# Kernel tuning notes

Hardware: AMD Instinct MI355X
Metric: run time of the kernel (lower is better)

## Reference

```python
import jax, jax.numpy as jnp
import numpy as np

EMBED_DIM = 1024
ATTN_DIM = 128
B, S = 4, 2048


def setup_inputs() -> dict:
    key = jax.random.key(0)
    k1, k2, k3, k4 = jax.random.split(key, 4)
    embedded = jax.random.normal(k1, (B, S, EMBED_DIM), dtype=jnp.float32)
    # torch nn.Linear weights are [out_features, in_features]
    scale = 1.0 / np.sqrt(EMBED_DIM)
    Wk = jax.random.uniform(k2, (ATTN_DIM, EMBED_DIM), dtype=jnp.float32, minval=-scale, maxval=scale)
    Wq = jax.random.uniform(k3, (ATTN_DIM, EMBED_DIM), dtype=jnp.float32, minval=-scale, maxval=scale)
    Wv = jax.random.uniform(k4, (ATTN_DIM, EMBED_DIM), dtype=jnp.float32, minval=-scale, maxval=scale)
    return {"embedded": embedded, "Wk": Wk, "Wq": Wq, "Wv": Wv}


def reference(embedded, Wk, Wq, Wv):
    # projections (no bias): x @ W.T
    k = jnp.einsum('bse,ae->bsa', embedded, Wk)  # [B,S,A]
    q = jnp.einsum('bse,ae->bsa', embedded, Wq)
    v = jnp.einsum('bse,ae->bsa', embedded, Wv)
    ad = k.shape[-1]
    scores = jnp.einsum('bqa,bka->bqk', q, k) / jnp.sqrt(jnp.float32(ad))  # [B,S,S]
    causal = jnp.tril(jnp.ones((scores.shape[1], scores.shape[1]), dtype=bool))
    scores = jnp.where(causal, scores, -jnp.inf)
    probs = jax.nn.softmax(scores, axis=-1)
    out = jnp.einsum('bqk,bka->bqa', probs, v)
    return jnp.round(out, 4)
```

## Files before the change

kernel.cpp:

```cpp
#include <hip/hip_runtime.h>
#include <hip/hip_bf16.h>
#include <math.h>

#define B 4
#define S 2048
#define E 1024
#define A 128
#define CHUNK 256
#define NCHMAX 8

typedef __attribute__((ext_vector_type(8))) short short8;
typedef __attribute__((ext_vector_type(4))) float floatx4;

static __device__ __forceinline__ short f2bf(float f) {
  union { float f; unsigned u; } c;
  c.f = f;
  unsigned r = (c.u + 0x7fffu + ((c.u >> 16) & 1u)) >> 16;
  return (short)r;
}
static __device__ __forceinline__ unsigned f2bf2(float x, float y) {
  __hip_bfloat162 h = __float22bfloat162_rn(float2{x, y});
  union { __hip_bfloat162 h; unsigned u; } c;
  c.h = h;
  return c.u;
}

__global__ __launch_bounds__(256) void wconv(
    const float* __restrict__ Wq,
    const float* __restrict__ Wk,
    const float* __restrict__ Wv,
    short* __restrict__ Wbf) {
  const int which = blockIdx.y;
  const float* Wp = (which == 0) ? Wq : (which == 1) ? Wk : Wv;
  short* o = Wbf + (size_t)which * A * E;
  const int f = blockIdx.x * 256 + threadIdx.x;
  const float4 v = *(const float4*)&Wp[(size_t)f * 4];
  uint2 p; p.x = f2bf2(v.x, v.y); p.y = f2bf2(v.z, v.w);
  *(uint2*)&o[(size_t)f * 4] = p;
}

#define PJ 72
__global__ __launch_bounds__(256) void proj_gemm(
    const float* __restrict__ X,
    const short* __restrict__ Wbf,
    short* __restrict__ Qbf,
    short* __restrict__ Kbf,
    short* __restrict__ Vt) {
  __shared__ short As[64 * PJ];
  __shared__ short Bs[128 * PJ];

  const int m0 = blockIdx.x * 64;
  const int which = blockIdx.y;
  const short* Wpb = Wbf + (size_t)which * A * E;

  const int tid = threadIdx.x;
  const int wave = tid >> 6;
  const int lane = tid & 63;
  const int mh = wave & 1;
  const int nh = wave >> 1;
  const int l16 = lane & 15;
  const int quad = lane >> 4;

  int arow[4], ac4[4], brow[4], bc8[4];
#pragma unroll
  for (int i = 0; i < 4; ++i) {
    const int fa = tid + i * 256;
    arow[i] = fa >> 4; ac4[i] = fa & 15;
    const int fb = tid + i * 256;
    brow[i] = fb >> 3; bc8[i] = fb & 7;
  }

  floatx4 acc[2][4] = {};
  float4 aplf[4];
  short8 bplf[4];

#pragma unroll
  for (int i = 0; i < 4; ++i) {
    aplf[i] = *(const float4*)&X[(size_t)(m0 + arow[i]) * E + ac4[i] * 4];
    bplf[i] = *(const short8*)&Wpb[(size_t)brow[i] * E + bc8[i] * 8];
  }

  for (int k0 = 0; k0 < E; k0 += 64) {
    __syncthreads();
#pragma unroll
    for (int i = 0; i < 4; ++i) {
      uint2 p; p.x = f2bf2(aplf[i].x, aplf[i].y); p.y = f2bf2(aplf[i].z, aplf[i].w);
      *(uint2*)&As[arow[i] * PJ + ac4[i] * 4] = p;
      *(short8*)&Bs[brow[i] * PJ + bc8[i] * 8] = bplf[i];
    }
    __syncthreads();

    if (k0 + 64 < E) {
#pragma unroll
      for (int i = 0; i < 4; ++i) {
        aplf[i] = *(const float4*)&X[(size_t)(m0 + arow[i]) * E + (k0 + 64) + ac4[i] * 4];
        bplf[i] = *(const short8*)&Wpb[(size_t)brow[i] * E + (k0 + 64) + bc8[i] * 8];
      }
    }

    short8 afr[2][2], bfr[4][2];
#pragma unroll
    for (int ms = 0; ms < 2; ++ms)
#pragma unroll
      for (int ks = 0; ks < 2; ++ks)
        afr[ms][ks] = *(const short8*)&As[(mh * 32 + ms * 16 + l16) * PJ + ks * 32 + quad * 8];
#pragma unroll
    for (int nt = 0; nt < 4; ++nt)
#pragma unroll
      for (int ks = 0; ks < 2; ++ks)
        bfr[nt][ks] = *(const short8*)&Bs[(nh * 64 + nt * 16 + l16) * PJ + ks * 32 + quad * 8];

#pragma unroll
    for (int ms = 0; ms < 2; ++ms)
#pragma unroll
      for (int nt = 0; nt < 4; ++nt)
#pragma unroll
        for (int ks = 0; ks < 2; ++ks)
          acc[ms][nt] = __builtin_amdgcn_mfma_f32_16x16x32_bf16(
              afr[ms][ks], bfr[nt][ks], acc[ms][nt], 0, 0, 0);
  }

  const float qscale = 0.08838834764831845f;
#pragma unroll
  for (int ms = 0; ms < 2; ++ms) {
#pragma unroll
    for (int nt = 0; nt < 4; ++nt) {
      const int n = nh * 64 + nt * 16 + l16;
      const int mbase = m0 + mh * 32 + ms * 16 + quad * 4;
      if (which == 2) {
        const int b = mbase >> 11, s = mbase & (S - 1);
        short4 p;
        p.x = f2bf(acc[ms][nt][0]); p.y = f2bf(acc[ms][nt][1]);
        p.z = f2bf(acc[ms][nt][2]); p.w = f2bf(acc[ms][nt][3]);
        *(short4*)&Vt[((size_t)b * A + n) * S + s] = p;
      } else {
        short* Outp = (which == 0) ? Qbf : Kbf;
        const float sc = (which == 0) ? qscale : 1.0f;
#pragma unroll
        for (int r = 0; r < 4; ++r)
          Outp[(size_t)(mbase + r) * A + n] = f2bf(acc[ms][nt][r] * sc);
      }
    }
  }
}

#define LK 132
#define LV 68
__global__ __launch_bounds__(256) void attn_part(
    const short* __restrict__ Qbf,
    const short* __restrict__ Kbf,
    const short* __restrict__ Vt,
    float* __restrict__ Opart,
    float* __restrict__ Lpart) {
  __shared__ short Ks[64 * LK];
  __shared__ short Vs[128 * LV];
  __shared__ short Ps[4][16 * LV];

  const int rev = (int)gridDim.x - 1 - (int)blockIdx.x;
  const int qt = rev >> 3;
  const int chunk = rev & 7;
  const int b = qt >> 5;
  const int q0 = (qt & 31) << 6;
  const int nk = q0 + 64;
  const int kstart = chunk * CHUNK;
  if (kstart >= nk) return;
  const int kend = min(kstart + CHUNK, nk);

  const int tid = threadIdx.x;
  const int wave = tid >> 6;
  const int lane = tid & 63;
  const int l16 = lane & 15;
  const int quad = lane >> 4;

  int krow[4], kc8[4], vrow[4], vc8[4];
#pragma unroll
  for (int i = 0; i < 4; ++i) {
    const int f = tid + i * 256;
    krow[i] = f >> 4; kc8[i] = f & 15;
    vrow[i] = f >> 3; vc8[i] = f & 7;
  }

  short8 qfr[4];
  {
    const size_t qrow = (size_t)(b * S + q0 + wave * 16 + l16);
#pragma unroll
    for (int ks = 0; ks < 4; ++ks)
      qfr[ks] = *(const short8*)&Qbf[qrow * A + ks * 32 + quad * 8];
  }

  float l_acc[4] = {0.f, 0.f, 0.f, 0.f};
  floatx4 oacc[8] = {};

  const int myrow = q0 + wave * 16 + quad * 4;
  const short* Kbase = Kbf + (size_t)b * S * A;
  const short* Vbase = Vt + (size_t)b * A * S;

  short8 kplf[4], vplf[4];
#pragma unroll
  for (int i = 0; i < 4; ++i) {
    kplf[i] = *(const short8*)&Kbase[(size_t)(kstart + krow[i]) * A + kc8[i] * 8];
    vplf[i] = *(const short8*)&Vbase[(size_t)vrow[i] * S + kstart + vc8[i] * 8];
  }

  for (int j0 = kstart; j0 < kend; j0 += 64) {
    __syncthreads();
#pragma unroll
    for (int i = 0; i < 4; ++i) {
      *(short8*)&Ks[krow[i] * LK + kc8[i] * 8] = kplf[i];
      *(short8*)&Vs[vrow[i] * LV + vc8[i] * 8] = vplf[i];
    }
    __syncthreads();

    if (j0 + 64 < kend) {
#pragma unroll
      for (int i = 0; i < 4; ++i) {
        kplf[i] = *(const short8*)&Kbase[(size_t)(j0 + 64 + krow[i]) * A + kc8[i] * 8];
        vplf[i] = *(const short8*)&Vbase[(size_t)vrow[i] * S + j0 + 64 + vc8[i] * 8];
      }
    }

    floatx4 sc[4];
#pragma unroll
    for (int nt = 0; nt < 4; ++nt) {
      floatx4 c = {};
#pragma unroll
      for (int ks = 0; ks < 4; ++ks) {
        const short8 bfr = *(const short8*)&Ks[(nt * 16 + l16) * LK + ks * 32 + quad * 8];
        c = __builtin_amdgcn_mfma_f32_16x16x32_bf16(qfr[ks], bfr, c, 0, 0, 0);
      }
      sc[nt] = c;
    }

#pragma unroll
    for (int nt = 0; nt < 4; ++nt) {
      const int key = j0 + nt * 16 + l16;
#pragma unroll
      for (int r = 0; r < 4; ++r) {
        const float p = (key > myrow + r) ? 0.f : __expf(sc[nt][r]);
        sc[nt][r] = p;
        l_acc[r] += p;
      }
    }

#pragma unroll
    for (int nt = 0; nt < 4; ++nt)
#pragma unroll
      for (int r = 0; r < 4; ++r)
        Ps[wave][(quad * 4 + r) * LV + nt * 16 + l16] = f2bf(sc[nt][r]);

    short8 pfr[2];
#pragma unroll
    for (int ks = 0; ks < 2; ++ks)
      pfr[ks] = *(const short8*)&Ps[wave][l16 * LV + ks * 32 + quad * 8];

#pragma unroll
    for (int nt = 0; nt < 8; ++nt) {
#pragma unroll
      for (int ks = 0; ks < 2; ++ks) {
        const short8 vfr = *(const short8*)&Vs[(nt * 16 + l16) * LV + ks * 32 + quad * 8];
        oacc[nt] = __builtin_amdgcn_mfma_f32_16x16x32_bf16(pfr[ks], vfr, oacc[nt], 0, 0, 0);
      }
    }
  }

  const int slot = qt * NCHMAX + chunk;
  float* op = Opart + (size_t)slot * 64 * 128;
  const int lr = wave * 16 + quad * 4;
#pragma unroll
  for (int nt = 0; nt < 8; ++nt)
#pragma unroll
    for (int r = 0; r < 4; ++r)
      op[(lr + r) * 128 + nt * 16 + l16] = oacc[nt][r];

#pragma unroll
  for (int r = 0; r < 4; ++r) {
    float l = l_acc[r];
    l += __shfl_xor(l, 1);
    l += __shfl_xor(l, 2);
    l += __shfl_xor(l, 4);
    l += __shfl_xor(l, 8);
    if (l16 == 0) Lpart[slot * 64 + lr + r] = l;
  }
}

__global__ __launch_bounds__(256) void attn_reduce(
    const float* __restrict__ Opart,
    const float* __restrict__ Lpart,
    float* __restrict__ Out) {
  const int qt = blockIdx.x;
  const int b = qt >> 5;
  const int q0 = (qt & 31) << 6;
  const int nch = (q0 + 64 + CHUNK - 1) / CHUNK;

  const int tid = threadIdx.x;
  const int lr = tid >> 2;
  const int c0 = (tid & 3) * 32;

  float ltot = 0.f;
  for (int c = 0; c < nch; ++c) ltot += Lpart[(qt * NCHMAX + c) * 64 + lr];
  const float inv = 1.f / ltot;

  float4 acc[8] = {};
  for (int c = 0; c < nch; ++c) {
    const float4* op = (const float4*)
        (Opart + ((size_t)(qt * NCHMAX + c) * 64 + lr) * 128 + c0);
#pragma unroll
    for (int i = 0; i < 8; ++i) {
      const float4 v = op[i];
      acc[i].x += v.x; acc[i].y += v.y; acc[i].z += v.z; acc[i].w += v.w;
    }
  }

  float4* o = (float4*)(Out + (size_t)(b * S + q0 + lr) * A + c0);
#pragma unroll
  for (int i = 0; i < 8; ++i) {
    float4 v = acc[i];
    v.x *= inv; v.y *= inv; v.z *= inv; v.w *= inv;
    o[i] = v;
  }
}

extern "C" void kernel_launch(void* const* d_in, const int* in_sizes, int n_in,
                              void* d_out, int out_size, void* d_ws, size_t ws_size,
                              hipStream_t stream) {
  const float* X  = (const float*)d_in[0];
  const float* Wk = (const float*)d_in[1];
  const float* Wq = (const float*)d_in[2];
  const float* Wv = (const float*)d_in[3];
  float* Out = (float*)d_out;

  const size_t qkv_elems = (size_t)B * S * A;
  short* Qbf = (short*)d_ws;
  short* Kbf = Qbf + qkv_elems;
  short* Vt  = Kbf + qkv_elems;
  float* Opart = (float*)(Vt + qkv_elems);
  float* Lpart = Opart + (size_t)1024 * 64 * 128;
  short* Wbf = (short*)(Lpart + (size_t)1024 * 64);

  wconv<<<dim3(A * E / 4 / 256, 3), 256, 0, stream>>>(Wq, Wk, Wv, Wbf);
  dim3 pgrid(B * S / 64, 3);
  proj_gemm<<<pgrid, 256, 0, stream>>>(X, Wbf, Qbf, Kbf, Vt);
  attn_part<<<(B * S / 64) * NCHMAX, 256, 0, stream>>>(Qbf, Kbf, Vt, Opart, Lpart);
  attn_reduce<<<B * S / 64, 256, 0, stream>>>(Opart, Lpart, Out);
}
```

Before: 131.5 us.

## Fuse split-K reduction into attention via last-block atomic counter; stage Q/K stores through LDS

Removes the separate attn_reduce kernel. Each attention chunk block increments a per-query-tile atomic counter, and the last block to finish sums the partial outputs and normalizes them. The projection GEMM now writes Q and K by staging the tile in shared memory, so the global stores become coalesced 16-byte writes instead of scattered 2-byte ones. The cost is an extra memset launch, threadfences and atomics, and a serialized reduction tail inside one block per tile.

New measurement: 361.4 us. +174.8%, slower.

```diff
diff --git a/kernel.cpp b/kernel.cpp
--- a/kernel.cpp
+++ b/kernel.cpp
@@ -40,14 +40,17 @@
 }
 
 #define PJ 72
+#define CN 130
 __global__ __launch_bounds__(256) void proj_gemm(
     const float* __restrict__ X,
     const short* __restrict__ Wbf,
     short* __restrict__ Qbf,
     short* __restrict__ Kbf,
     short* __restrict__ Vt) {
-  __shared__ short As[64 * PJ];
-  __shared__ short Bs[128 * PJ];
+  __shared__ __align__(16) char smem[27648];
+  short* As = (short*)smem;
+  short* Bs = (short*)(smem + 9216);
+  short* Cs = (short*)smem;
 
   const int m0 = blockIdx.x * 64;
   const int which = blockIdx.y;
@@ -121,25 +124,39 @@
   }
 
   const float qscale = 0.08838834764831845f;
-#pragma unroll
-  for (int ms = 0; ms < 2; ++ms) {
-#pragma unroll
-    for (int nt = 0; nt < 4; ++nt) {
-      const int n = nh * 64 + nt * 16 + l16;
-      const int mbase = m0 + mh * 32 + ms * 16 + quad * 4;
-      if (which == 2) {
+  if (which == 2) {
+#pragma unroll
+    for (int ms = 0; ms < 2; ++ms) {
+#pragma unroll
+      for (int nt = 0; nt < 4; ++nt) {
+        const int n = nh * 64 + nt * 16 + l16;
+        const int mbase = m0 + mh * 32 + ms * 16 + quad * 4;
         const int b = mbase >> 11, s = mbase & (S - 1);
         short4 p;
         p.x = f2bf(acc[ms][nt][0]); p.y = f2bf(acc[ms][nt][1]);
         p.z = f2bf(acc[ms][nt][2]); p.w = f2bf(acc[ms][nt][3]);
         *(short4*)&Vt[((size_t)b * A + n) * S + s] = p;
-      } else {
-        short* Outp = (which == 0) ? Qbf : Kbf;
-        const float sc = (which == 0) ? qscale : 1.0f;
+      }
+    }
+  } else {
+    __syncthreads();
+    const float sc = (which == 0) ? qscale : 1.0f;
+#pragma unroll
+    for (int ms = 0; ms < 2; ++ms)
+#pragma unroll
+      for (int nt = 0; nt < 4; ++nt)
 #pragma unroll
         for (int r = 0; r < 4; ++r)
-          Outp[(size_t)(mbase + r) * A + n] = f2bf(acc[ms][nt][r] * sc);
-      }
+          Cs[(mh * 32 + ms * 16 + quad * 4 + r) * CN + nh * 64 + nt * 16 + l16] =
+              f2bf(acc[ms][nt][r] * sc);
+    __syncthreads();
+    short* Outp = (which == 0) ? Qbf : Kbf;
+#pragma unroll
+    for (int i = 0; i < 4; ++i) {
+      const int f = tid + i * 256;
+      const int row = f >> 4, c8 = f & 15;
+      *(short8*)&Outp[(size_t)(m0 + row) * A + c8 * 8] =
+          *(const short8*)&Cs[row * CN + c8 * 8];
     }
   }
 }
@@ -151,10 +168,13 @@
     const short* __restrict__ Kbf,
     const short* __restrict__ Vt,
     float* __restrict__ Opart,
-    float* __restrict__ Lpart) {
+    float* __restrict__ Lpart,
+    unsigned* __restrict__ Cnt,
+    float* __restrict__ Out) {
   __shared__ short Ks[64 * LK];
   __shared__ short Vs[128 * LV];
   __shared__ short Ps[4][16 * LV];
+  __shared__ unsigned lastflag;
 
   const int rev = (int)gridDim.x - 1 - (int)blockIdx.x;
   const int qt = rev >> 3;
@@ -165,6 +185,7 @@
   const int kstart = chunk * CHUNK;
   if (kstart >= nk) return;
   const int kend = min(kstart + CHUNK, nk);
+  const int nch = (nk + CHUNK - 1) / CHUNK;
 
   const int tid = threadIdx.x;
   const int wave = tid >> 6;
@@ -265,12 +286,12 @@
 
   const int slot = qt * NCHMAX + chunk;
   float* op = Opart + (size_t)slot * 64 * 128;
-  const int lr = wave * 16 + quad * 4;
+  const int lr4 = wave * 16 + quad * 4;
 #pragma unroll
   for (int nt = 0; nt < 8; ++nt)
 #pragma unroll
     for (int r = 0; r < 4; ++r)
-      op[(lr + r) * 128 + nt * 16 + l16] = oacc[nt][r];
+      op[(lr4 + r) * 128 + nt * 16 + l16] = oacc[nt][r];
 
 #pragma unroll
   for (int r = 0; r < 4; ++r) {
@@ -279,20 +300,16 @@
     l += __shfl_xor(l, 2);
     l += __shfl_xor(l, 4);
     l += __shfl_xor(l, 8);
-    if (l16 == 0) Lpart[slot * 64 + lr + r] = l;
-  }
-}
-
-__global__ __launch_bounds__(256) void attn_reduce(
-    const float* __restrict__ Opart,
-    const float* __restrict__ Lpart,
-    float* __restrict__ Out) {
-  const int qt = blockIdx.x;
-  const int b = qt >> 5;
-  const int q0 = (qt & 31) << 6;
-  const int nch = (q0 + 64 + CHUNK - 1) / CHUNK;
-
-  const int tid = threadIdx.x;
+    if (l16 == 0) Lpart[slot * 64 + lr4 + r] = l;
+  }
+
+  __threadfence();
+  __syncthreads();
+  if (tid == 0) lastflag = atomicAdd(&Cnt[qt], 1u);
+  __syncthreads();
+  if (lastflag != (unsigned)(nch - 1)) return;
+  __threadfence();
+
   const int lr = tid >> 2;
   const int c0 = (tid & 3) * 32;
 
@@ -300,21 +317,20 @@
   for (int c = 0; c < nch; ++c) ltot += Lpart[(qt * NCHMAX + c) * 64 + lr];
   const float inv = 1.f / ltot;
 
-  float4 acc[8] = {};
+  float4 racc[8] = {};
   for (int c = 0; c < nch; ++c) {
-    const float4* op = (const float4*)
+    const float4* rp = (const float4*)
         (Opart + ((size_t)(qt * NCHMAX + c) * 64 + lr) * 128 + c0);
 #pragma unroll
     for (int i = 0; i < 8; ++i) {
-      const float4 v = op[i];
-      acc[i].x += v.x; acc[i].y += v.y; acc[i].z += v.z; acc[i].w += v.w;
-    }
-  }
-
+      const float4 v = rp[i];
+      racc[i].x += v.x; racc[i].y += v.y; racc[i].z += v.z; racc[i].w += v.w;
+    }
+  }
   float4* o = (float4*)(Out + (size_t)(b * S + q0 + lr) * A + c0);
 #pragma unroll
   for (int i = 0; i < 8; ++i) {
-    float4 v = acc[i];
+    float4 v = racc[i];
     v.x *= inv; v.y *= inv; v.z *= inv; v.w *= inv;
     o[i] = v;
   }
@@ -336,10 +352,12 @@
   float* Opart = (float*)(Vt + qkv_elems);
   float* Lpart = Opart + (size_t)1024 * 64 * 128;
   short* Wbf = (short*)(Lpart + (size_t)1024 * 64);
+  unsigned* Cnt = (unsigned*)(Wbf + (size_t)3 * A * E);
+
+  hipMemsetAsync(Cnt, 0, 128 * sizeof(unsigned), stream);
 
   wconv<<<dim3(A * E / 4 / 256, 3), 256, 0, stream>>>(Wq, Wk, Wv, Wbf);
   dim3 pgrid(B * S / 64, 3);
   proj_gemm<<<pgrid, 256, 0, stream>>>(X, Wbf, Qbf, Kbf, Vt);
-  attn_part<<<(B * S / 64) * NCHMAX, 256, 0, stream>>>(Qbf, Kbf, Vt, Opart, Lpart);
-  attn_reduce<<<B * S / 64, 256, 0, stream>>>(Opart, Lpart, Out);
-}
+  attn_part<<<(B * S / 64) * NCHMAX, 256, 0, stream>>>(Qbf, Kbf, Vt, Opart, Lpart, Cnt, Out);
+}
```
